# Kernel optimization log

Hardware: AMD Instinct MI355X
Metric: run time of the kernel (lower is better)

The kernel has to match this reference:

```python
import jax, jax.numpy as jnp
import numpy as np

CELL = 8
POS_MARGIN = 1.0
NEG_MARGIN = 0.2
LAMBDA_D = 250.0
LAMBDA_LOSS = 0.0001


def _resize_bilinear(x, out_h, out_w):
    # torch F.interpolate(..., mode='bilinear', align_corners=False) half-pixel sampling
    B, H, W = x.shape
    def axis(n_in, n_out):
        src = (jnp.arange(n_out, dtype=jnp.float32) + 0.5) * (n_in / n_out) - 0.5
        src = jnp.clip(src, 0.0, n_in - 1.0)
        i0 = jnp.floor(src).astype(jnp.int32)
        i1 = jnp.minimum(i0 + 1, n_in - 1)
        w = src - i0.astype(jnp.float32)
        return i0, i1, w
    r0, r1, wr = axis(H, out_h)
    xr = x[:, r0, :] * (1.0 - wr)[None, :, None] + x[:, r1, :] * wr[None, :, None]
    c0, c1, wc = axis(W, out_w)
    return xr[:, :, c0] * (1.0 - wc)[None, None, :] + xr[:, :, c1] * wc[None, None, :]


def detector_loss(pred, heatmap, vm):
    eps = 1e-7
    pos_inds = (heatmap == 1.0).astype(pred.dtype)
    neg_inds = (heatmap < 1.0).astype(pred.dtype)
    neg_weights = (1.0 - heatmap) ** 4
    num_pos = pos_inds.sum()
    pos_loss = (jnp.log(pred + eps) * (1.0 - pred) ** 2 * pos_inds * vm).sum()
    neg_loss = (jnp.log(1.0 - pred + eps) * pred ** 2 * neg_weights * neg_inds * vm).sum()
    return jnp.where(num_pos == 0, -neg_loss, -(pos_loss + neg_loss) / jnp.maximum(num_pos, 1.0))


def descriptor_loss(desc, wdesc, Hmat, vm, wvm):
    B, D, Hc, Wc = desc.shape
    N = Hc * Wc
    # cell-center coordinates in (row=y, col=x) order
    ii, jj = np.meshgrid(np.arange(Hc), np.arange(Wc), indexing='ij')
    coords = (np.stack([ii, jj], axis=-1) * CELL + CELL // 2).astype(np.float32)  # [Hc,Wc,2]
    coords = jnp.asarray(coords)
    pts = coords.reshape(-1, 2)
    # warp points with homographies (convert (y,x) -> (x,y), apply H, convert back)
    H_list = Hmat[:, 0]  # [B,3,3]
    homog = jnp.concatenate([pts[:, ::-1], jnp.ones((N, 1), jnp.float32)], axis=-1)  # [N,3]
    w = jnp.einsum('bij,nj->bni', H_list, homog)
    warped = (w[..., :2] / w[..., 2:3])[..., ::-1]  # back to (y,x), [B,N,2]
    warped = warped.reshape(B, Hc, Wc, 1, 1, 2)
    cell_dist = jnp.linalg.norm(coords.reshape(1, 1, 1, Hc, Wc, 2) - warped, axis=-1)  # [B,Hc,Wc,Hc,Wc]
    s = (cell_dist <= CELL - 0.5).astype(jnp.float32)

    normalization = wvm.sum()
    vm_c = _resize_bilinear(vm, Hc, Wc) > 0.5
    wvm_c = _resize_bilinear(wvm, Hc, Wc) > 0.5
    valid_pair = (vm_c.reshape(B, Hc, Wc, 1, 1) & wvm_c.reshape(B, 1, 1, Hc, Wc)).astype(jnp.float32)

    def l2norm(x):
        return x / jnp.maximum(jnp.linalg.norm(x, axis=-1, keepdims=True), 1e-12)

    d = l2norm(jnp.transpose(desc, (0, 2, 3, 1)))    # [B,Hc,Wc,D]
    wd = l2norm(jnp.transpose(wdesc, (0, 2, 3, 1)))  # [B,Hc,Wc,D]
    dot = jnp.einsum('bijd,bkld->bijkl', d, wd)      # all-pairs cosine sim
    dot = jax.nn.relu(dot)
    positive_dist = jnp.maximum(0.0, POS_MARGIN - dot)
    negative_dist = jnp.maximum(0.0, dot - NEG_MARGIN)
    loss = (LAMBDA_D * s * positive_dist + (1.0 - s) * negative_dist) * valid_pair
    return loss.sum() / normalization


def setup_inputs() -> dict:
    key = jax.random.key(0)
    ks = jax.random.split(key, 8)
    B, H, W, D, Hc, Wc = 2, 480, 640, 256, 60, 80
    Hmat = jnp.eye(3, dtype=jnp.float32)[None, None] + 0.05 * jax.random.normal(ks[6], (B, 1, 3, 3), jnp.float32)
    return {
        'prob': jax.random.uniform(ks[0], (B, H, W), jnp.float32),
        'ht': jax.random.uniform(ks[1], (B, H, W), jnp.float32),
        'valid_mask': jnp.ones((B, H, W), jnp.float32),
        'warped_prob': jax.random.uniform(ks[2], (B, H, W), jnp.float32),
        'warped_ht': jax.random.uniform(ks[3], (B, H, W), jnp.float32),
        'warped_valid_mask': jnp.ones((B, H, W), jnp.float32),
        'desc_raw': jax.random.normal(ks[4], (B, D, Hc, Wc), jnp.float32),
        'warped_desc_raw': jax.random.normal(ks[5], (B, D, Hc, Wc), jnp.float32),
        'Hmat': Hmat,
    }


def reference(prob, ht, valid_mask, warped_prob, warped_ht, warped_valid_mask, desc_raw, warped_desc_raw, Hmat):
    points_loss = detector_loss(prob, ht, valid_mask)
    warped_points_loss = detector_loss(warped_prob, warped_ht, warped_valid_mask)
    desc_loss = descriptor_loss(desc_raw, warped_desc_raw, Hmat, valid_mask, warped_valid_mask)
    total = points_loss + warped_points_loss + LAMBDA_LOSS * desc_loss
    return total, points_loss, warped_points_loss, desc_loss
```

## Files before the change

### kernel.cpp

```cpp
#include <hip/hip_runtime.h>
#include <hip/hip_bf16.h>
#include <cmath>

#define BB 2
#define HH 480
#define WW 640
#define DD 256
#define HC 60
#define WC 80
#define NN (HC*WC)

#define DET_BLOCKS 300

#define NTILES64 (NN/64)
#define DESC_BLOCKS_F32 (BB*NTILES64*NTILES64)
#define TS3 96
#define BK 32
#define NT96 (NN/TS3)
#define BLK96 (NT96*NT96)
#define GEMM_BLOCKS (BB*BLK96)
#define CORR_BLOCKS (BB*NN/4)
#define DESC_GRID (GEMM_BLOCKS + CORR_BLOCKS)

#define OFF_DET0  0
#define OFF_DET1  2048
#define OFF_INVA  16384
#define OFF_INVB  (OFF_INVA + BB*NN)
#define OFF_WRW   (OFF_INVB + BB*NN)
#define OFF_WCL   (OFF_WRW + BB*NN)
#define OFF_VMC   (OFF_WCL + BB*NN)
#define OFF_WVMC  (OFF_VMC + BB*NN)
#define OFF_SQP   (OFF_WVMC + BB*NN)
#define OFF_DESCP (OFF_SQP + 16*NN)
#define OFF_TA    172032
#define TA_FLOATS (BB*NN*DD/2)
#define OFF_TB    (OFF_TA + TA_FLOATS)
#define WS_NEED   ((size_t)(OFF_TB + TA_FLOATS) * 4)

typedef __attribute__((ext_vector_type(8))) short short8;
typedef __attribute__((ext_vector_type(4))) float f32x4;

__device__ inline float bf2f(unsigned short u)
{
    unsigned int x = ((unsigned int)u) << 16;
    return __builtin_bit_cast(float, x);
}

__device__ inline void det_accum(float p, float h, float v,
                                 float& posl, float& negl, float& npos, float& vsum)
{
    float omp = 1.f - p;
    if (h == 1.0f) {
        posl += logf(p + 1e-7f) * omp*omp * v;
        npos += 1.f;
    }
    if (h < 1.0f) {
        float oh = 1.f - h;
        float w4 = oh*oh; w4 *= w4;
        negl += logf(omp + 1e-7f) * p*p * w4 * v;
    }
    vsum += v;
}

__global__ __launch_bounds__(256) void det_kernel(
    const float* __restrict__ pred0, const float* __restrict__ hmap0, const float* __restrict__ vm0,
    const float* __restrict__ pred1, const float* __restrict__ hmap1, const float* __restrict__ vm1,
    float* __restrict__ ws)
{
    const int set = blockIdx.y;
    const float4* pred = (const float4*)(set ? pred1 : pred0);
    const float4* hmap = (const float4*)(set ? hmap1 : hmap0);
    const float4* vm   = (const float4*)(set ? vm1   : vm0);
    float* partials = ws + (set ? OFF_DET1 : OFF_DET0);

    float posl = 0.f, negl = 0.f, npos = 0.f, vsum = 0.f;
    const int total4 = BB*HH*WW/4;
    for (int i = blockIdx.x*256 + threadIdx.x; i < total4; i += DET_BLOCKS*256) {
        float4 p = pred[i], h = hmap[i], v = vm[i];
        det_accum(p.x, h.x, v.x, posl, negl, npos, vsum);
        det_accum(p.y, h.y, v.y, posl, negl, npos, vsum);
        det_accum(p.z, h.z, v.z, posl, negl, npos, vsum);
        det_accum(p.w, h.w, v.w, posl, negl, npos, vsum);
    }
    __shared__ float red[256];
    int t = threadIdx.x;
    float vals[4] = {posl, negl, npos, vsum};
    for (int j = 0; j < 4; ++j) {
        red[t] = vals[j]; __syncthreads();
        for (int s = 128; s > 0; s >>= 1) { if (t < s) red[t] += red[t+s]; __syncthreads(); }
        if (t == 0) partials[blockIdx.x*4 + j] = red[0];
        __syncthreads();
    }
}

__global__ __launch_bounds__(256) void sumsq_kernel(
    const float* __restrict__ desc, const float* __restrict__ wdesc,
    float* __restrict__ ws)
{
    const int n = blockIdx.x*256 + threadIdx.x;
    if (n >= NN) return;
    const int dc = blockIdx.y;
    const int z  = blockIdx.z;
    const float* src = ((z & 1) ? wdesc : desc) + (size_t)(z >> 1)*DD*NN;
    float s = 0.f;
    const int d0 = dc*64;
    #pragma unroll 8
    for (int d = d0; d < d0 + 64; ++d) {
        float v = src[(size_t)d*NN + n];
        s = fmaf(v, v, s);
    }
    ws[OFF_SQP + ((size_t)z*4 + dc)*NN + n] = s;
}

__device__ inline float bilin_cell(const float* __restrict__ x, int i, int j)
{
    float sr = (i + 0.5f) * ((float)HH/(float)HC) - 0.5f;
    sr = fminf(fmaxf(sr, 0.f), (float)(HH-1));
    int r0 = (int)floorf(sr); int r1 = min(r0+1, HH-1); float wr = sr - (float)r0;
    float sc = (j + 0.5f) * ((float)WW/(float)WC) - 0.5f;
    sc = fminf(fmaxf(sc, 0.f), (float)(WW-1));
    int c0 = (int)floorf(sc); int c1 = min(c0+1, WW-1); float wc = sc - (float)c0;
    float v00 = x[r0*WW+c0], v01 = x[r0*WW+c1];
    float v10 = x[r1*WW+c0], v11 = x[r1*WW+c1];
    float e0 = v00*(1.f-wr) + v10*wr;
    float e1 = v01*(1.f-wr) + v11*wr;
    return e0*(1.f-wc) + e1*wc;
}

__device__ inline void prep_geom(int idx, const float* __restrict__ vm,
                                 const float* __restrict__ wvm,
                                 const float* __restrict__ Hmat, float* __restrict__ ws)
{
    int b = idx / NN, n = idx % NN;
    int i = n / WC, j = n % WC;
    float px = (float)(j*8 + 4), py = (float)(i*8 + 4);
    const float* Hb = Hmat + b*9;
    float w0 = Hb[0]*px + Hb[1]*py + Hb[2];
    float w1 = Hb[3]*px + Hb[4]*py + Hb[5];
    float w2 = Hb[6]*px + Hb[7]*py + Hb[8];
    ws[OFF_WRW + idx] = w1 / w2;
    ws[OFF_WCL + idx] = w0 / w2;
    ws[OFF_VMC  + idx] = (bilin_cell(vm  + (size_t)b*HH*WW, i, j) > 0.5f) ? 1.f : 0.f;
    ws[OFF_WVMC + idx] = (bilin_cell(wvm + (size_t)b*HH*WW, i, j) > 0.5f) ? 1.f : 0.f;
}

__global__ __launch_bounds__(256) void prep_kernel(
    const float* __restrict__ vm, const float* __restrict__ wvm,
    const float* __restrict__ Hmat, float* __restrict__ ws)
{
    int idx = blockIdx.x*256 + threadIdx.x;
    if (idx >= BB*NN) return;
    int b = idx / NN, n = idx % NN;

    const float* sq = ws + OFF_SQP;
    float sa = 0.f, sb = 0.f;
    #pragma unroll
    for (int k = 0; k < 4; ++k) {
        sa += sq[((b*2+0)*4 + k)*NN + n];
        sb += sq[((b*2+1)*4 + k)*NN + n];
    }
    ws[OFF_INVA + idx] = 1.f / fmaxf(sqrtf(sa), 1e-12f);
    ws[OFF_INVB + idx] = 1.f / fmaxf(sqrtf(sb), 1e-12f);
    prep_geom(idx, vm, wvm, Hmat, ws);
}

__global__ __launch_bounds__(256) void prep_kernel_full(
    const float* __restrict__ desc, const float* __restrict__ wdesc,
    const float* __restrict__ vm, const float* __restrict__ wvm,
    const float* __restrict__ Hmat, float* __restrict__ ws)
{
    int idx = blockIdx.x*256 + threadIdx.x;
    if (idx >= BB*NN) return;
    int b = idx / NN, n = idx % NN;

    const float* a  = desc  + (size_t)b*DD*NN + n;
    const float* bp = wdesc + (size_t)b*DD*NN + n;
    float sa = 0.f, sb = 0.f;
    for (int d = 0; d < DD; ++d) {
        float x = a[(size_t)d*NN];  sa = fmaf(x, x, sa);
        float y = bp[(size_t)d*NN]; sb = fmaf(y, y, sb);
    }
    ws[OFF_INVA + idx] = 1.f / fmaxf(sqrtf(sa), 1e-12f);
    ws[OFF_INVB + idx] = 1.f / fmaxf(sqrtf(sb), 1e-12f);
    prep_geom(idx, vm, wvm, Hmat, ws);
}

__global__ __launch_bounds__(256) void transpose_kernel(
    const float* __restrict__ desc, const float* __restrict__ wdesc,
    unsigned short* __restrict__ ta, unsigned short* __restrict__ tb,
    const float* __restrict__ ws)
{
    const int nb = blockIdx.x * 64;
    const int db = blockIdx.y * 64;
    const int z  = blockIdx.z;
    const int b  = z >> 1;
    const float* src = (z & 1) ? wdesc : desc;
    unsigned short* dst = (z & 1) ? tb : ta;
    src += (size_t)b*DD*NN;
    dst += (size_t)b*NN*DD;

    __shared__ float tile[64][65];
    const int tr = threadIdx.x >> 6;
    const int tc = threadIdx.x & 63;
    #pragma unroll
    for (int i = 0; i < 16; ++i) {
        int d = db + i*4 + tr;
        tile[i*4 + tr][tc] = src[(size_t)d*NN + nb + tc];
    }
    __syncthreads();
    const int idxn = b*NN + nb + tc;
    const float scl = (z & 1) ? ws[OFF_INVB + idxn] * ws[OFF_WVMC + idxn]
                              : ws[OFF_INVA + idxn] * ws[OFF_VMC  + idxn];
    #pragma unroll
    for (int gg = 0; gg < 2; ++gg) {
        int g = tr + gg*4;
        short8 v8;
        #pragma unroll
        for (int j = 0; j < 8; ++j) {
            float v = tile[g*8 + j][tc] * scl;
            __hip_bfloat16 h = __float2bfloat16(v);
            v8[j] = (short)__builtin_bit_cast(unsigned short, h);
        }
        int sg = (db >> 3) + g;
        *(short8*)(dst + ((size_t)sg*NN + nb + tc)*8) = v8;
    }
}

__global__ __launch_bounds__(256) void desc_mfma(
    const unsigned short* __restrict__ ta, const unsigned short* __restrict__ tb,
    const float* __restrict__ ws, float* __restrict__ partials)
{
    __shared__ unsigned short As[2][TS3*BK];
    __shared__ unsigned short Bs[2][TS3*BK];
    __shared__ float corr_red[4];

    const int bidx = blockIdx.x;
    const int tid  = threadIdx.x;
    const int lane = tid & 63;
    const int wid  = tid >> 6;

    if (bidx < CORR_BLOCKS) {
        const int idx = bidx*4 + wid;
        const int cb  = idx / NN, cn = idx % NN;
        const float wrow = ws[OFF_WRW + idx];
        const float wcol = ws[OFF_WCL + idx];
        const float va   = ws[OFF_VMC + idx];
        const unsigned short* tA = ta + (size_t)cb*NN*DD;
        const unsigned short* tB = tb + (size_t)cb*NN*DD;
        const float* wvmc = ws + OFF_WVMC + cb*NN;

        const int sg = lane >> 1;
        const int e  = (lane & 1) * 4;
        const unsigned short* ap = tA + ((size_t)sg*NN + cn)*8 + e;
        float a0 = bf2f(ap[0]), a1 = bf2f(ap[1]), a2 = bf2f(ap[2]), a3 = bf2f(ap[3]);

        const int ibase = (int)floorf((wrow - 4.f) * 0.125f);
        const int jbase = (int)floorf((wcol - 4.f) * 0.125f);
        float corr = 0.f;
        #pragma unroll
        for (int di = 0; di < 2; ++di) {
            #pragma unroll
            for (int dj = 0; dj < 2; ++dj) {
                int ii = ibase + di, jj = jbase + dj;
                float dr = (float)(ii*8 + 4) - wrow;
                float dc = (float)(jj*8 + 4) - wcol;
                bool ok = (ii >= 0) && (ii < HC) && (jj >= 0) && (jj < WC)
                          && (dr*dr + dc*dc) <= 56.25f;
                if (ok) {
                    int m = ii*WC + jj;
                    const unsigned short* bp = tB + ((size_t)sg*NN + m)*8 + e;
                    float d = a0*bf2f(bp[0]);
                    d = fmaf(a1, bf2f(bp[1]), d);
                    d = fmaf(a2, bf2f(bp[2]), d);
                    d = fmaf(a3, bf2f(bp[3]), d);
                    #pragma unroll
                    for (int off = 1; off < 64; off <<= 1)
                        d += __shfl_xor(d, off, 64);
                    float dotr = fmaxf(d, 0.f);
                    float pos = 250.f * fmaxf(1.f - dotr, 0.f);
                    float neg = fmaxf(d - 0.2f, 0.f);
                    corr += (pos - neg) * va * wvmc[m];
                }
            }
        }
        if (lane == 0) corr_red[wid] = corr;
        __syncthreads();
        if (tid == 0)
            partials[bidx] = corr_red[0] + corr_red[1] + corr_red[2] + corr_red[3];
        return;
    }

    const int g   = bidx - CORR_BLOCKS;
    const int swz = (g & 7) * (GEMM_BLOCKS/8) + (g >> 3);
    const int b   = swz / BLK96;
    const int rr  = swz % BLK96;
    const int n0  = (rr / NT96) * TS3;
    const int m0  = (rr % NT96) * TS3;

    const int wr = wid >> 1, wc = wid & 1;
    const unsigned short* tab = ta + (size_t)b*NN*DD;
    const unsigned short* tbb = tb + (size_t)b*NN*DD;

#define STAGE(t_, buf_)                                                          \
    {                                                                            \
        _Pragma("unroll")                                                        \
        for (int c = 0; c < 3; ++c) {                                            \
            int c2 = wid*3 + c;                                                  \
            int cA = (c2 < 6) ? c2 : (c2 - 6);                                   \
            int o  = cA*64 + lane;                                               \
            int s  = o / TS3;                                                    \
            int r  = o - s*TS3;                                                  \
            const unsigned short* gp = (c2 < 6)                                  \
                ? (tab + ((size_t)((t_)*4 + s)*NN + n0 + r)*8)                   \
                : (tbb + ((size_t)((t_)*4 + s)*NN + m0 + r)*8);                  \
            unsigned short* l0 = (c2 < 6) ? &As[buf_][cA*512] : &Bs[buf_][cA*512];\
            __builtin_amdgcn_global_load_lds(                                    \
                (const __attribute__((address_space(1))) void*)gp,               \
                (__attribute__((address_space(3))) void*)l0, 16, 0, 0);          \
        }                                                                        \
    }

    const int ln15   = lane & 15;
    const int slot16 = lane >> 4;
    f32x4 acc[3][3] = {};

    STAGE(0, 0);

    #pragma unroll
    for (int t = 0; t < 8; ++t) {
        if (t < 7) STAGE(t+1, (t+1)&1);
        if (t < 7) asm volatile("s_waitcnt vmcnt(3)" ::: "memory");
        else       asm volatile("s_waitcnt vmcnt(0)" ::: "memory");
        __builtin_amdgcn_s_barrier();
        __builtin_amdgcn_sched_barrier(0);
        const unsigned short* Ab = As[t&1];
        const unsigned short* Bb = Bs[t&1];
        short8 af[3], bf[3];
        #pragma unroll
        for (int f = 0; f < 3; ++f) {
            int ra = wr*48 + f*16 + ln15;
            af[f] = *(const short8*)(Ab + (slot16*TS3 + ra)*8);
            int rb = wc*48 + f*16 + ln15;
            bf[f] = *(const short8*)(Bb + (slot16*TS3 + rb)*8);
        }
        #pragma unroll
        for (int fi = 0; fi < 3; ++fi)
            #pragma unroll
            for (int fj = 0; fj < 3; ++fj)
                acc[fi][fj] = __builtin_amdgcn_mfma_f32_16x16x32_bf16(
                    af[fi], bf[fj], acc[fi][fj], 0, 0, 0);
        __builtin_amdgcn_sched_barrier(0);
        __builtin_amdgcn_s_barrier();
    }

    float sum = 0.f;
    #pragma unroll
    for (int fi = 0; fi < 3; ++fi)
        #pragma unroll
        for (int fj = 0; fj < 3; ++fj)
            #pragma unroll
            for (int reg = 0; reg < 4; ++reg)
                sum += fmaxf(acc[fi][fj][reg] - 0.2f, 0.f);

    float* red = (float*)&As[0][0];
    red[tid] = sum; __syncthreads();
    for (int s = 128; s > 0; s >>= 1) { if (tid < s) red[tid] += red[tid+s]; __syncthreads(); }
    if (tid == 0) partials[bidx] = red[0];
#undef STAGE
}

__global__ __launch_bounds__(256) void desc_kernel(
    const float* __restrict__ desc, const float* __restrict__ wdesc,
    const float* __restrict__ ws, float* __restrict__ partials)
{
    const int b  = blockIdx.z;
    const int n0 = blockIdx.y * 64;
    const int m0 = blockIdx.x * 64;
    const float* A  = desc  + (size_t)b*DD*NN;
    const float* Bm = wdesc + (size_t)b*DD*NN;

    __shared__ float As[32][64];
    __shared__ float Bs[32][64];

    const int tid = threadIdx.x;
    const int tx = tid & 15, ty = tid >> 4;
    float acc[4][4] = {{0.f}};

    for (int k0 = 0; k0 < DD; k0 += 32) {
        #pragma unroll
        for (int l = 0; l < 8; ++l) {
            int e = tid + l*256;
            int kk = e >> 6, nn = e & 63;
            As[kk][nn] = A [(size_t)(k0+kk)*NN + n0 + nn];
            Bs[kk][nn] = Bm[(size_t)(k0+kk)*NN + m0 + nn];
        }
        __syncthreads();
        #pragma unroll
        for (int kk = 0; kk < 32; ++kk) {
            float4 av = *reinterpret_cast<const float4*>(&As[kk][ty*4]);
            float4 bv = *reinterpret_cast<const float4*>(&Bs[kk][tx*4]);
            float a4[4] = {av.x, av.y, av.z, av.w};
            float b4[4] = {bv.x, bv.y, bv.z, bv.w};
            #pragma unroll
            for (int r = 0; r < 4; ++r)
                #pragma unroll
                for (int c = 0; c < 4; ++c)
                    acc[r][c] = fmaf(a4[r], b4[c], acc[r][c]);
        }
        __syncthreads();
    }

    const float* inva = ws + OFF_INVA + b*NN;
    const float* invb = ws + OFF_INVB + b*NN;
    const float* wrp  = ws + OFF_WRW + b*NN;
    const float* wcp  = ws + OFF_WCL + b*NN;
    const float* vmc  = ws + OFF_VMC + b*NN;
    const float* wvmc = ws + OFF_WVMC + b*NN;

    int nb = n0 + ty*4, mb = m0 + tx*4;
    float ia[4], wrv[4], wcv[4], va[4];
    #pragma unroll
    for (int r = 0; r < 4; ++r) {
        int n = nb + r;
        ia[r] = inva[n]; wrv[r] = wrp[n]; wcv[r] = wcp[n]; va[r] = vmc[n];
    }
    float ib[4], vb[4], crow[4], ccol[4];
    #pragma unroll
    for (int c = 0; c < 4; ++c) {
        int m = mb + c;
        ib[c] = invb[m]; vb[c] = wvmc[m];
        crow[c] = (float)((m / WC)*8 + 4);
        ccol[c] = (float)((m % WC)*8 + 4);
    }
    float sum = 0.f;
    #pragma unroll
    for (int r = 0; r < 4; ++r) {
        #pragma unroll
        for (int c = 0; c < 4; ++c) {
            float dot = fmaxf(acc[r][c] * ia[r] * ib[c], 0.f);
            float dr = crow[c] - wrv[r];
            float dc = ccol[c] - wcv[r];
            bool s = (dr*dr + dc*dc) <= 56.25f;
            float term = s ? 250.f * fmaxf(1.f - dot, 0.f)
                           : fmaxf(dot - 0.2f, 0.f);
            sum += term * va[r] * vb[c];
        }
    }

    __shared__ float red[256];
    red[tid] = sum; __syncthreads();
    for (int s = 128; s > 0; s >>= 1) { if (tid < s) red[tid] += red[tid+s]; __syncthreads(); }
    if (tid == 0) {
        int bid = (blockIdx.z * gridDim.y + blockIdx.y) * gridDim.x + blockIdx.x;
        partials[bid] = red[0];
    }
}

__global__ __launch_bounds__(256) void finalize_kernel(
    const float* __restrict__ ws, float* __restrict__ out, int desc_nblocks)
{
    __shared__ float red[256];
    int t = threadIdx.x;
    float res[2];
    float norm = 0.f;
    for (int pass = 0; pass < 2; ++pass) {
        const float* p = ws + (pass == 0 ? OFF_DET0 : OFF_DET1);
        float s0=0.f, s1=0.f, s2=0.f, s3=0.f;
        for (int i = t; i < DET_BLOCKS; i += 256) {
            s0 += p[i*4+0]; s1 += p[i*4+1]; s2 += p[i*4+2]; s3 += p[i*4+3];
        }
        float v[4] = {s0,s1,s2,s3};
        float tot[4];
        for (int j = 0; j < 4; ++j) {
            red[t] = v[j]; __syncthreads();
            for (int s = 128; s > 0; s >>= 1) { if (t < s) red[t] += red[t+s]; __syncthreads(); }
            tot[j] = red[0]; __syncthreads();
        }
        float posl = tot[0], negl = tot[1], npos = tot[2], vsum = tot[3];
        res[pass] = (npos == 0.f) ? -negl : -(posl + negl) / fmaxf(npos, 1.f);
        if (pass == 1) norm = vsum;
    }
    float ds = 0.f;
    for (int i = t; i < desc_nblocks; i += 256) ds += ws[OFF_DESCP + i];
    red[t] = ds; __syncthreads();
    for (int s = 128; s > 0; s >>= 1) { if (t < s) red[t] += red[t+s]; __syncthreads(); }
    float descsum = red[0];
    if (t == 0) {
        float desc_loss = descsum / norm;
        float total = res[0] + res[1] + 1e-4f * desc_loss;
        out[0] = total;
        out[1] = res[0];
        out[2] = res[1];
        out[3] = desc_loss;
    }
}

extern "C" void kernel_launch(void* const* d_in, const int* in_sizes, int n_in,
                              void* d_out, int out_size, void* d_ws, size_t ws_size,
                              hipStream_t stream)
{
    const float* prob  = (const float*)d_in[0];
    const float* htm   = (const float*)d_in[1];
    const float* vmask = (const float*)d_in[2];
    const float* wprob = (const float*)d_in[3];
    const float* wht   = (const float*)d_in[4];
    const float* wvm   = (const float*)d_in[5];
    const float* desc  = (const float*)d_in[6];
    const float* wdesc = (const float*)d_in[7];
    const float* Hm    = (const float*)d_in[8];
    float* ws  = (float*)d_ws;
    float* out = (float*)d_out;

    det_kernel<<<dim3(DET_BLOCKS, 2), 256, 0, stream>>>(
        prob, htm, vmask, wprob, wht, wvm, ws);

    if (ws_size >= WS_NEED) {
        unsigned short* ta = (unsigned short*)(ws + OFF_TA);
        unsigned short* tb = (unsigned short*)(ws + OFF_TB);
        sumsq_kernel<<<dim3((NN + 255)/256, 4, 4), 256, 0, stream>>>(desc, wdesc, ws);
        prep_kernel<<<(BB*NN + 255)/256, 256, 0, stream>>>(vmask, wvm, Hm, ws);
        transpose_kernel<<<dim3(NN/64, DD/64, BB*2), 256, 0, stream>>>(desc, wdesc, ta, tb, ws);
        desc_mfma<<<DESC_GRID, 256, 0, stream>>>(ta, tb, ws, ws + OFF_DESCP);
        finalize_kernel<<<1, 256, 0, stream>>>(ws, out, DESC_GRID);
    } else {
        prep_kernel_full<<<(BB*NN + 255)/256, 256, 0, stream>>>(desc, wdesc, vmask, wvm, Hm, ws);
        desc_kernel<<<dim3(NTILES64, NTILES64, BB), 256, 0, stream>>>(desc, wdesc, ws, ws + OFF_DESCP);
        finalize_kernel<<<1, 256, 0, stream>>>(ws, out, DESC_BLOCKS_F32);
    }
}
```

Baseline: 71.47 us.

## Triple-buffer desc GEMM LDS pipeline and fuse detector with sumsq kernel

The bf16 MFMA GEMM moves from double to triple LDS buffering. It now issues two stages ahead, places the next prefetch after the fragment reads, and drops the trailing barrier, so each k-step has one barrier instead of two. Separately, the detector-loss reduction and the descriptor sum-of-squares kernel are merged into one launch, with the grid split by block index, which removes a launch and lets both memory-bound jobs share the GPU. The extra LDS buffer raises shared memory per block, which may lower occupancy, and the single-barrier scheme relies on careful ordering between buffer reuse and vmcnt waits.

Result: faster. 67.53 us (-5.5%).

```diff
diff --git a/kernel.cpp b/kernel.cpp
--- a/kernel.cpp
+++ b/kernel.cpp
@@ -11,6 +11,8 @@
 #define NN (HC*WC)
 
 #define DET_BLOCKS 300
+#define SUMSQ_NB ((NN + 255)/256)
+#define P0_BLOCKS (2*DET_BLOCKS + 16*SUMSQ_NB)
 
 #define NTILES64 (NN/64)
 #define DESC_BLOCKS_F32 (BB*NTILES64*NTILES64)
@@ -62,12 +64,34 @@
     vsum += v;
 }
 
-__global__ __launch_bounds__(256) void det_kernel(
+__global__ __launch_bounds__(256) void det_sumsq_kernel(
     const float* __restrict__ pred0, const float* __restrict__ hmap0, const float* __restrict__ vm0,
     const float* __restrict__ pred1, const float* __restrict__ hmap1, const float* __restrict__ vm1,
+    const float* __restrict__ desc, const float* __restrict__ wdesc,
     float* __restrict__ ws)
 {
-    const int set = blockIdx.y;
+    const int bidx = blockIdx.x;
+    if (bidx >= 2*DET_BLOCKS) {
+        const int sid   = bidx - 2*DET_BLOCKS;
+        const int combo = sid / SUMSQ_NB;
+        const int nb    = sid % SUMSQ_NB;
+        const int z  = combo >> 2;
+        const int dc = combo & 3;
+        const int n  = nb*256 + threadIdx.x;
+        if (n >= NN) return;
+        const float* src = ((z & 1) ? wdesc : desc) + (size_t)(z >> 1)*DD*NN;
+        float s = 0.f;
+        const int d0 = dc*64;
+        #pragma unroll 8
+        for (int d = d0; d < d0 + 64; ++d) {
+            float v = src[(size_t)d*NN + n];
+            s = fmaf(v, v, s);
+        }
+        ws[OFF_SQP + ((size_t)z*4 + dc)*NN + n] = s;
+        return;
+    }
+    const int set = bidx / DET_BLOCKS;
+    const int db  = bidx % DET_BLOCKS;
     const float4* pred = (const float4*)(set ? pred1 : pred0);
     const float4* hmap = (const float4*)(set ? hmap1 : hmap0);
     const float4* vm   = (const float4*)(set ? vm1   : vm0);
@@ -75,7 +99,7 @@
 
     float posl = 0.f, negl = 0.f, npos = 0.f, vsum = 0.f;
     const int total4 = BB*HH*WW/4;
-    for (int i = blockIdx.x*256 + threadIdx.x; i < total4; i += DET_BLOCKS*256) {
+    for (int i = db*256 + threadIdx.x; i < total4; i += DET_BLOCKS*256) {
         float4 p = pred[i], h = hmap[i], v = vm[i];
         det_accum(p.x, h.x, v.x, posl, negl, npos, vsum);
         det_accum(p.y, h.y, v.y, posl, negl, npos, vsum);
@@ -88,28 +112,9 @@
     for (int j = 0; j < 4; ++j) {
         red[t] = vals[j]; __syncthreads();
         for (int s = 128; s > 0; s >>= 1) { if (t < s) red[t] += red[t+s]; __syncthreads(); }
-        if (t == 0) partials[blockIdx.x*4 + j] = red[0];
+        if (t == 0) partials[db*4 + j] = red[0];
         __syncthreads();
     }
-}
-
-__global__ __launch_bounds__(256) void sumsq_kernel(
-    const float* __restrict__ desc, const float* __restrict__ wdesc,
-    float* __restrict__ ws)
-{
-    const int n = blockIdx.x*256 + threadIdx.x;
-    if (n >= NN) return;
-    const int dc = blockIdx.y;
-    const int z  = blockIdx.z;
-    const float* src = ((z & 1) ? wdesc : desc) + (size_t)(z >> 1)*DD*NN;
-    float s = 0.f;
-    const int d0 = dc*64;
-    #pragma unroll 8
-    for (int d = d0; d < d0 + 64; ++d) {
-        float v = src[(size_t)d*NN + n];
-        s = fmaf(v, v, s);
-    }
-    ws[OFF_SQP + ((size_t)z*4 + dc)*NN + n] = s;
 }
 
 __device__ inline float bilin_cell(const float* __restrict__ x, int i, int j)
@@ -230,8 +235,8 @@
     const unsigned short* __restrict__ ta, const unsigned short* __restrict__ tb,
     const float* __restrict__ ws, float* __restrict__ partials)
 {
-    __shared__ unsigned short As[2][TS3*BK];
-    __shared__ unsigned short Bs[2][TS3*BK];
+    __shared__ unsigned short As[3][TS3*BK];
+    __shared__ unsigned short Bs[3][TS3*BK];
     __shared__ float corr_red[4];
 
     const int bidx = blockIdx.x;
@@ -297,7 +302,6 @@
     const int n0  = (rr / NT96) * TS3;
     const int m0  = (rr % NT96) * TS3;
 
-    const int wr = wid >> 1, wc = wid & 1;
     const unsigned short* tab = ta + (size_t)b*NN*DD;
     const unsigned short* tbb = tb + (size_t)b*NN*DD;
 
@@ -320,21 +324,22 @@
         }                                                                        \
     }
 
+    const int wr = wid >> 1, wc = wid & 1;
     const int ln15   = lane & 15;
     const int slot16 = lane >> 4;
     f32x4 acc[3][3] = {};
 
     STAGE(0, 0);
+    STAGE(1, 1);
 
     #pragma unroll
     for (int t = 0; t < 8; ++t) {
-        if (t < 7) STAGE(t+1, (t+1)&1);
         if (t < 7) asm volatile("s_waitcnt vmcnt(3)" ::: "memory");
         else       asm volatile("s_waitcnt vmcnt(0)" ::: "memory");
         __builtin_amdgcn_s_barrier();
         __builtin_amdgcn_sched_barrier(0);
-        const unsigned short* Ab = As[t&1];
-        const unsigned short* Bb = Bs[t&1];
+        const unsigned short* Ab = As[t % 3];
+        const unsigned short* Bb = Bs[t % 3];
         short8 af[3], bf[3];
         #pragma unroll
         for (int f = 0; f < 3; ++f) {
@@ -343,14 +348,13 @@
             int rb = wc*48 + f*16 + ln15;
             bf[f] = *(const short8*)(Bb + (slot16*TS3 + rb)*8);
         }
+        if (t < 6) STAGE(t+2, (t+2) % 3);
         #pragma unroll
         for (int fi = 0; fi < 3; ++fi)
             #pragma unroll
             for (int fj = 0; fj < 3; ++fj)
                 acc[fi][fj] = __builtin_amdgcn_mfma_f32_16x16x32_bf16(
                     af[fi], bf[fj], acc[fi][fj], 0, 0, 0);
-        __builtin_amdgcn_sched_barrier(0);
-        __builtin_amdgcn_s_barrier();
     }
 
     float sum = 0.f;
@@ -511,18 +515,18 @@
     float* ws  = (float*)d_ws;
     float* out = (float*)d_out;
 
-    det_kernel<<<dim3(DET_BLOCKS, 2), 256, 0, stream>>>(
-        prob, htm, vmask, wprob, wht, wvm, ws);
-
     if (ws_size >= WS_NEED) {
         unsigned short* ta = (unsigned short*)(ws + OFF_TA);
         unsigned short* tb = (unsigned short*)(ws + OFF_TB);
-        sumsq_kernel<<<dim3((NN + 255)/256, 4, 4), 256, 0, stream>>>(desc, wdesc, ws);
+        det_sumsq_kernel<<<P0_BLOCKS, 256, 0, stream>>>(
+            prob, htm, vmask, wprob, wht, wvm, desc, wdesc, ws);
         prep_kernel<<<(BB*NN + 255)/256, 256, 0, stream>>>(vmask, wvm, Hm, ws);
         transpose_kernel<<<dim3(NN/64, DD/64, BB*2), 256, 0, stream>>>(desc, wdesc, ta, tb, ws);
         desc_mfma<<<DESC_GRID, 256, 0, stream>>>(ta, tb, ws, ws + OFF_DESCP);
         finalize_kernel<<<1, 256, 0, stream>>>(ws, out, DESC_GRID);
     } else {
+        det_sumsq_kernel<<<2*DET_BLOCKS, 256, 0, stream>>>(
+            prob, htm, vmask, wprob, wht, wvm, desc, wdesc, ws);
         prep_kernel_full<<<(BB*NN + 255)/256, 256, 0, stream>>>(desc, wdesc, vmask, wvm, Hm, ws);
         desc_kernel<<<dim3(NTILES64, NTILES64, BB), 256, 0, stream>>>(desc, wdesc, ws, ws + OFF_DESCP);
         finalize_kernel<<<1, 256, 0, stream>>>(ws, out, DESC_BLOCKS_F32);
```
